# Kernel optimization log

Hardware: AMD Instinct MI355X
Metric: run time of the kernel (lower is better)

The kernel has to match this reference:

```python
import jax, jax.numpy as jnp
import numpy as np

N, TO, TI, H = 8, 2048, 2048, 128
MASK_FILL = -99999.0  # module uses -99999.0, not -inf


def setup_inputs() -> dict:
    key = jax.random.key(0)
    kq, kv, km = jax.random.split(key, 3)
    queries = jax.random.normal(kq, (N, TO, H), dtype=jnp.float32)
    values = jax.random.normal(kv, (N, TI, H), dtype=jnp.float32)
    # mask is applied to scores.view(-1, Ti) -> shape (N*To, Ti), True = masked
    mask = jax.random.randint(km, (N * TO, TI), 0, 2).astype(bool)
    return {"queries": queries, "values": values, "mask": mask}


def reference(queries, values, mask):
    n, to, h = queries.shape
    ti = values.shape[1]
    # N x To x Ti scores (no 1/sqrt(H) scaling in the original)
    scores = jnp.einsum("nth,nsh->nts", queries, values)
    scores = jnp.where(mask.reshape(n, to, ti), MASK_FILL, scores)
    attention_distribution = jax.nn.softmax(scores, axis=-1)
    attention_output = jnp.einsum("nts,nsh->nth", attention_distribution, values)
    return attention_output, attention_distribution
```

## Files before the change

kernel.cpp:

```cpp
#include <hip/hip_runtime.h>

#define NB  8
#define TOQ 2048
#define TIV 2048
#define HD  128

typedef float f32x4 __attribute__((ext_vector_type(4)));
typedef short s16x8 __attribute__((ext_vector_type(8)));
typedef unsigned short ushort8v __attribute__((ext_vector_type(8)));

__device__ __forceinline__ unsigned short f2bf(float f) {
    unsigned u = __float_as_uint(f);
    return (unsigned short)((u + 0x7FFFu + ((u >> 16) & 1u)) >> 16);
}
__device__ __forceinline__ float bf2f(unsigned short h) {
    return __uint_as_float(((unsigned)h) << 16);
}

__device__ __forceinline__ void split8(const float4 a, const float4 b,
                                       ushort8v& h, ushort8v& l) {
    const float x[8] = {a.x, a.y, a.z, a.w, b.x, b.y, b.z, b.w};
    #pragma unroll
    for (int j = 0; j < 8; ++j) {
        const unsigned short hi = f2bf(x[j]);
        h[j] = hi;
        l[j] = f2bf(x[j] - bf2f(hi));
    }
}

__global__ __launch_bounds__(256) void k0_vt(
    const float* __restrict__ V, unsigned short* __restrict__ VT)
{
    __shared__ unsigned short tile[64][68];
    const int n  = blockIdx.z;
    const int s0 = blockIdx.x * 64;
    const int h0 = blockIdx.y * 64;
    const int t  = threadIdx.x;

    #pragma unroll
    for (int it = 0; it < 4; ++it) {
        const int f = t + it * 256;
        const int r = f >> 4;
        const int c = f & 15;
        const float4 v = *(const float4*)&V[((size_t)(n * TIV + s0 + r)) * HD + h0 + 4 * c];
        tile[4 * c + 0][r] = f2bf(v.x);
        tile[4 * c + 1][r] = f2bf(v.y);
        tile[4 * c + 2][r] = f2bf(v.z);
        tile[4 * c + 3][r] = f2bf(v.w);
    }
    __syncthreads();

    #pragma unroll
    for (int it = 0; it < 2; ++it) {
        const int f  = t + it * 256;
        const int hh = f >> 3;
        const int sc = f & 7;
        ushort8v o;
        #pragma unroll
        for (int j = 0; j < 8; ++j) o[j] = tile[hh][8 * sc + j];
        *(ushort8v*)&VT[((size_t)(n * HD + h0 + hh)) * TIV + s0 + 8 * sc] = o;
    }
}

__global__ __launch_bounds__(256) void k1_mfma(
    const float* __restrict__ Q, const float* __restrict__ V,
    const int* __restrict__ M, float* __restrict__ E)
{
    __shared__ unsigned short qhi[128 * 32], qlo[128 * 32];
    __shared__ unsigned short vhi[128 * 32], vlo[128 * 32];

    const int n    = blockIdx.z;
    const int tt   = blockIdx.y * 128;
    const int ts   = blockIdx.x * 128;
    const int t    = threadIdx.x;
    const int lane = t & 63;
    const int wave = t >> 6;
    const int wr   = wave >> 1;
    const int wc   = wave & 1;
    const int lr   = lane & 15;
    const int kg   = lane >> 4;

    const float* Qb = Q + ((size_t)n * TOQ + tt) * HD;
    const float* Vb = V + ((size_t)n * TIV + ts) * HD;

    f32x4 acc[4][4];
    #pragma unroll
    for (int i = 0; i < 4; ++i)
        #pragma unroll
        for (int j = 0; j < 4; ++j) acc[i][j] = (f32x4)0.f;

    for (int h0 = 0; h0 < HD; h0 += 32) {
        #pragma unroll
        for (int it = 0; it < 2; ++it) {
            const int i   = t + it * 256;
            const int row = i >> 2;
            const int kb  = i & 3;
            const float* qs = Qb + (size_t)row * HD + h0 + kb * 8;
            const float* vs = Vb + (size_t)row * HD + h0 + kb * 8;
            const float4 q0 = *(const float4*)qs, q1 = *(const float4*)(qs + 4);
            const float4 v0 = *(const float4*)vs, v1 = *(const float4*)(vs + 4);
            ushort8v qh, ql, vh, vl;
            split8(q0, q1, qh, ql);
            split8(v0, v1, vh, vl);
            *(ushort8v*)(qhi + i * 8) = qh;
            *(ushort8v*)(qlo + i * 8) = ql;
            *(ushort8v*)(vhi + i * 8) = vh;
            *(ushort8v*)(vlo + i * 8) = vl;
        }
        __syncthreads();

        s16x8 aH[4], aL[4];
        #pragma unroll
        for (int fm = 0; fm < 4; ++fm) {
            const int off = (wr * 64 + fm * 16 + lr) * 32 + kg * 8;
            aH[fm] = *(const s16x8*)(qhi + off);
            aL[fm] = *(const s16x8*)(qlo + off);
        }
        #pragma unroll
        for (int fn = 0; fn < 4; ++fn) {
            const int off = (wc * 64 + fn * 16 + lr) * 32 + kg * 8;
            const s16x8 bH = *(const s16x8*)(vhi + off);
            const s16x8 bL = *(const s16x8*)(vlo + off);
            #pragma unroll
            for (int fm = 0; fm < 4; ++fm) {
                acc[fm][fn] = __builtin_amdgcn_mfma_f32_16x16x32_bf16(aH[fm], bH, acc[fm][fn], 0, 0, 0);
                acc[fm][fn] = __builtin_amdgcn_mfma_f32_16x16x32_bf16(aH[fm], bL, acc[fm][fn], 0, 0, 0);
                acc[fm][fn] = __builtin_amdgcn_mfma_f32_16x16x32_bf16(aL[fm], bH, acc[fm][fn], 0, 0, 0);
            }
        }
        __syncthreads();
    }

    #pragma unroll
    for (int fm = 0; fm < 4; ++fm) {
        #pragma unroll
        for (int fn = 0; fn < 4; ++fn) {
            #pragma unroll
            for (int ri = 0; ri < 4; ++ri) {
                const int r = tt + wr * 64 + fm * 16 + kg * 4 + ri;
                const int c = ts + wc * 64 + fn * 16 + lr;
                const size_t off = ((size_t)n * TOQ + r) * TIV + c;
                E[off] = M[off] ? 0.f : __expf(acc[fm][fn][ri]);
            }
        }
    }
}

__global__ __launch_bounds__(256) void k2_rowsum(
    const float* __restrict__ E, float* __restrict__ rec)
{
    const int row = blockIdx.x * 4 + (threadIdx.x >> 6);
    const int l   = threadIdx.x & 63;
    const float4* Er = (const float4*)(E + (size_t)row * TIV);
    float s = 0.f;
    #pragma unroll
    for (int k = 0; k < 8; ++k) {
        const float4 v = Er[l + 64 * k];
        s += (v.x + v.y) + (v.z + v.w);
    }
    #pragma unroll
    for (int off = 32; off > 0; off >>= 1) s += __shfl_down(s, off, 64);
    if (l == 0) rec[row] = 1.f / s;
}

__global__ __launch_bounds__(512) void k3_pv(
    float* EP,
    const unsigned short* __restrict__ VT,
    const float* __restrict__ rec, float* __restrict__ O)
{
    __shared__ float red[4][16][132];

    const int n    = blockIdx.y;
    const int r0   = blockIdx.x * 64;
    const int t    = threadIdx.x;
    const int wave = t >> 6;
    const int lane = t & 63;
    const int p    = wave >> 1;
    const int half = wave & 1;
    const int lr   = lane & 15;
    const int kg   = lane >> 4;

    const int rowg = r0 + p * 16 + lr;
    const float rc = rec[n * TOQ + rowg];
    float* Erow = EP + ((size_t)n * TOQ + rowg) * TIV;
    const unsigned short* VTb = VT + (size_t)n * HD * TIV;

    f32x4 acc[8];
    #pragma unroll
    for (int fn = 0; fn < 8; ++fn) acc[fn] = (f32x4)0.f;

    const int kbase = half * 1024 + kg * 8;

    #pragma unroll 2
    for (int k0 = 0; k0 < 1024; k0 += 32) {
        const int k = kbase + k0;
        const float4 e0 = *(const float4*)&Erow[k];
        const float4 e1 = *(const float4*)&Erow[k + 4];
        float4 p0, p1;
        p0.x = e0.x * rc; p0.y = e0.y * rc; p0.z = e0.z * rc; p0.w = e0.w * rc;
        p1.x = e1.x * rc; p1.y = e1.y * rc; p1.z = e1.z * rc; p1.w = e1.w * rc;
        *(float4*)&Erow[k]     = p0;
        *(float4*)&Erow[k + 4] = p1;

        s16x8 a;
        a[0] = (short)f2bf(p0.x); a[1] = (short)f2bf(p0.y);
        a[2] = (short)f2bf(p0.z); a[3] = (short)f2bf(p0.w);
        a[4] = (short)f2bf(p1.x); a[5] = (short)f2bf(p1.y);
        a[6] = (short)f2bf(p1.z); a[7] = (short)f2bf(p1.w);

        #pragma unroll
        for (int fn = 0; fn < 8; ++fn) {
            const s16x8 b = *(const s16x8*)&VTb[(size_t)(fn * 16 + lr) * TIV + k];
            acc[fn] = __builtin_amdgcn_mfma_f32_16x16x32_bf16(a, b, acc[fn], 0, 0, 0);
        }
    }

    if (half == 1) {
        #pragma unroll
        for (int fn = 0; fn < 8; ++fn)
            #pragma unroll
            for (int ri = 0; ri < 4; ++ri)
                red[p][kg * 4 + ri][fn * 16 + lr] = acc[fn][ri];
    }
    __syncthreads();
    if (half == 0) {
        #pragma unroll
        for (int fn = 0; fn < 8; ++fn) {
            #pragma unroll
            for (int ri = 0; ri < 4; ++ri) {
                const int orow = r0 + p * 16 + kg * 4 + ri;
                const float o = acc[fn][ri] + red[p][kg * 4 + ri][fn * 16 + lr];
                O[((size_t)n * TOQ + orow) * HD + fn * 16 + lr] = o;
            }
        }
    }
}

extern "C" void kernel_launch(void* const* d_in, const int* in_sizes, int n_in,
                              void* d_out, int out_size, void* d_ws, size_t ws_size,
                              hipStream_t stream)
{
    const float* Q = (const float*)d_in[0];
    const float* V = (const float*)d_in[1];
    const int*   M = (const int*)d_in[2];

    float* O = (float*)d_out;
    float* E = O + (size_t)NB * TOQ * HD;

    float*          recb = (float*)d_ws;
    unsigned short* VT   = (unsigned short*)((char*)d_ws + (1 << 16));

    k0_vt    <<<dim3(TIV / 64, HD / 64, NB), 256, 0, stream>>>(V, VT);
    k1_mfma  <<<dim3(TIV / 128, TOQ / 128, NB), 256, 0, stream>>>(Q, V, M, E);
    k2_rowsum<<<dim3(NB * TOQ / 4), 256, 0, stream>>>(E, recb);
    k3_pv    <<<dim3(TOQ / 64, NB), 512, 0, stream>>>(E, VT, recb, O);
}
```

Before: 198.0 us.

## Fuse row-sum partials into score kernel and split PV K-range four ways

The score kernel now accumulates per-row partial sums of the exponentials and writes 32 partials per row to workspace. The row-sum kernel then reduces those partials instead of re-reading the full 128MB exp matrix. The PV kernel processes 32 rows per block with four waves splitting the K range, which doubles the number of blocks, and reduces the partial results through shared memory. This removes a full pass over E in exchange for a small partials buffer and more shared-memory reduction work.

```diff
diff --git a/kernel.cpp b/kernel.cpp
--- a/kernel.cpp
+++ b/kernel.cpp
@@ -64,7 +64,8 @@
 
 __global__ __launch_bounds__(256) void k1_mfma(
     const float* __restrict__ Q, const float* __restrict__ V,
-    const int* __restrict__ M, float* __restrict__ E)
+    const int* __restrict__ M, float* __restrict__ E,
+    float* __restrict__ part)
 {
     __shared__ unsigned short qhi[128 * 32], qlo[128 * 32];
     __shared__ unsigned short vhi[128 * 32], vlo[128 * 32];
@@ -131,6 +132,12 @@
         __syncthreads();
     }
 
+    float rsum[4][4];
+    #pragma unroll
+    for (int fm = 0; fm < 4; ++fm)
+        #pragma unroll
+        for (int ri = 0; ri < 4; ++ri) rsum[fm][ri] = 0.f;
+
     #pragma unroll
     for (int fm = 0; fm < 4; ++fm) {
         #pragma unroll
@@ -140,43 +147,56 @@
                 const int r = tt + wr * 64 + fm * 16 + kg * 4 + ri;
                 const int c = ts + wc * 64 + fn * 16 + lr;
                 const size_t off = ((size_t)n * TOQ + r) * TIV + c;
-                E[off] = M[off] ? 0.f : __expf(acc[fm][fn][ri]);
+                const float e = M[off] ? 0.f : __expf(acc[fm][fn][ri]);
+                E[off] = e;
+                rsum[fm][ri] += e;
+            }
+        }
+    }
+    #pragma unroll
+    for (int fm = 0; fm < 4; ++fm) {
+        #pragma unroll
+        for (int ri = 0; ri < 4; ++ri) {
+            float s = rsum[fm][ri];
+            s += __shfl_xor(s, 1, 64);
+            s += __shfl_xor(s, 2, 64);
+            s += __shfl_xor(s, 4, 64);
+            s += __shfl_xor(s, 8, 64);
+            if (lr == 0) {
+                const int r = tt + wr * 64 + fm * 16 + kg * 4 + ri;
+                part[((size_t)n * TOQ + r) * 32 + blockIdx.x * 2 + wc] = s;
             }
         }
     }
 }
 
 __global__ __launch_bounds__(256) void k2_rowsum(
-    const float* __restrict__ E, float* __restrict__ rec)
-{
-    const int row = blockIdx.x * 4 + (threadIdx.x >> 6);
-    const int l   = threadIdx.x & 63;
-    const float4* Er = (const float4*)(E + (size_t)row * TIV);
+    const float* __restrict__ part, float* __restrict__ rec)
+{
+    const int row = blockIdx.x * 256 + threadIdx.x;
+    const float4* p4 = (const float4*)(part + (size_t)row * 32);
     float s = 0.f;
     #pragma unroll
-    for (int k = 0; k < 8; ++k) {
-        const float4 v = Er[l + 64 * k];
+    for (int i = 0; i < 8; ++i) {
+        const float4 v = p4[i];
         s += (v.x + v.y) + (v.z + v.w);
     }
-    #pragma unroll
-    for (int off = 32; off > 0; off >>= 1) s += __shfl_down(s, off, 64);
-    if (l == 0) rec[row] = 1.f / s;
+    rec[row] = 1.f / s;
 }
 
 __global__ __launch_bounds__(512) void k3_pv(
-    float* EP,
-    const unsigned short* __restrict__ VT,
+    float* __restrict__ EP, const unsigned short* __restrict__ VT,
     const float* __restrict__ rec, float* __restrict__ O)
 {
-    __shared__ float red[4][16][132];
+    __shared__ float red[2][3][16][132];
 
     const int n    = blockIdx.y;
-    const int r0   = blockIdx.x * 64;
+    const int r0   = blockIdx.x * 32;
     const int t    = threadIdx.x;
     const int wave = t >> 6;
     const int lane = t & 63;
-    const int p    = wave >> 1;
-    const int half = wave & 1;
+    const int p    = wave >> 2;
+    const int q    = wave & 3;
     const int lr   = lane & 15;
     const int kg   = lane >> 4;
 
@@ -189,10 +209,10 @@
     #pragma unroll
     for (int fn = 0; fn < 8; ++fn) acc[fn] = (f32x4)0.f;
 
-    const int kbase = half * 1024 + kg * 8;
+    const int kbase = q * 512 + kg * 8;
 
     #pragma unroll 2
-    for (int k0 = 0; k0 < 1024; k0 += 32) {
+    for (int k0 = 0; k0 < 512; k0 += 32) {
         const int k = kbase + k0;
         const float4 e0 = *(const float4*)&Erow[k];
         const float4 e1 = *(const float4*)&Erow[k + 4];
@@ -215,21 +235,24 @@
         }
     }
 
-    if (half == 1) {
+    if (q != 0) {
         #pragma unroll
         for (int fn = 0; fn < 8; ++fn)
             #pragma unroll
             for (int ri = 0; ri < 4; ++ri)
-                red[p][kg * 4 + ri][fn * 16 + lr] = acc[fn][ri];
+                red[p][q - 1][kg * 4 + ri][fn * 16 + lr] = acc[fn][ri];
     }
     __syncthreads();
-    if (half == 0) {
+    if (q == 0) {
         #pragma unroll
         for (int fn = 0; fn < 8; ++fn) {
             #pragma unroll
             for (int ri = 0; ri < 4; ++ri) {
                 const int orow = r0 + p * 16 + kg * 4 + ri;
-                const float o = acc[fn][ri] + red[p][kg * 4 + ri][fn * 16 + lr];
+                float o = acc[fn][ri];
+                o += red[p][0][kg * 4 + ri][fn * 16 + lr];
+                o += red[p][1][kg * 4 + ri][fn * 16 + lr];
+                o += red[p][2][kg * 4 + ri][fn * 16 + lr];
                 O[((size_t)n * TOQ + orow) * HD + fn * 16 + lr] = o;
             }
         }
@@ -248,10 +271,11 @@
     float* E = O + (size_t)NB * TOQ * HD;
 
     float*          recb = (float*)d_ws;
-    unsigned short* VT   = (unsigned short*)((char*)d_ws + (1 << 16));
+    float*          part = (float*)((char*)d_ws + (1 << 16));
+    unsigned short* VT   = (unsigned short*)((char*)d_ws + (1 << 16) + (NB * TOQ * 32 * 4));
 
     k0_vt    <<<dim3(TIV / 64, HD / 64, NB), 256, 0, stream>>>(V, VT);
-    k1_mfma  <<<dim3(TIV / 128, TOQ / 128, NB), 256, 0, stream>>>(Q, V, M, E);
-    k2_rowsum<<<dim3(NB * TOQ / 4), 256, 0, stream>>>(E, recb);
-    k3_pv    <<<dim3(TOQ / 64, NB), 512, 0, stream>>>(E, VT, recb, O);
-}
+    k1_mfma  <<<dim3(TIV / 128, TOQ / 128, NB), 256, 0, stream>>>(Q, V, M, E, part);
+    k2_rowsum<<<dim3(NB * TOQ / 256), 256, 0, stream>>>(part, recb);
+    k3_pv    <<<dim3(TOQ / 32, NB), 512, 0, stream>>>(E, VT, recb, O);
+}
```

Result: faster. 188.0 us (-5.0%).

## Store unnormalized exp scores as bf16 in-place and split PV reduction four ways

Applied to the files above, without the earlier changes.

The score kernel now writes exp(scores) as bf16 into the first half of each fp32 row of the output buffer, which halves the intermediate write and the row-sum read traffic. The PV kernel preloads a whole bf16 row segment into registers, syncs, then overwrites the row with normalized fp32 probabilities so the in-place aliasing stays safe. Work is split into four K-quarters per 16-row group with a larger shared-memory reduction, and blocks cover 32 rows instead of 64. In exchange, the attention distribution loses precision because it is rebuilt from bf16 exponentials, and register pressure rises from the 16-element preload buffer.

```diff
diff --git a/kernel.cpp b/kernel.cpp
--- a/kernel.cpp
+++ b/kernel.cpp
@@ -64,7 +64,7 @@
 
 __global__ __launch_bounds__(256) void k1_mfma(
     const float* __restrict__ Q, const float* __restrict__ V,
-    const int* __restrict__ M, float* __restrict__ E)
+    const int* __restrict__ M, float* __restrict__ Pf)
 {
     __shared__ unsigned short qhi[128 * 32], qlo[128 * 32];
     __shared__ unsigned short vhi[128 * 32], vlo[128 * 32];
@@ -139,74 +139,83 @@
             for (int ri = 0; ri < 4; ++ri) {
                 const int r = tt + wr * 64 + fm * 16 + kg * 4 + ri;
                 const int c = ts + wc * 64 + fn * 16 + lr;
-                const size_t off = ((size_t)n * TOQ + r) * TIV + c;
-                E[off] = M[off] ? 0.f : __expf(acc[fm][fn][ri]);
+                const size_t R   = (size_t)n * TOQ + r;
+                const size_t off = R * TIV + c;
+                unsigned short* Eu = (unsigned short*)(Pf + R * TIV);
+                Eu[c] = M[off] ? (unsigned short)0 : f2bf(__expf(acc[fm][fn][ri]));
             }
         }
     }
 }
 
 __global__ __launch_bounds__(256) void k2_rowsum(
-    const float* __restrict__ E, float* __restrict__ rec)
+    const float* __restrict__ Pf, float* __restrict__ rec)
 {
     const int row = blockIdx.x * 4 + (threadIdx.x >> 6);
     const int l   = threadIdx.x & 63;
-    const float4* Er = (const float4*)(E + (size_t)row * TIV);
+    const unsigned short* Eu = (const unsigned short*)(Pf + (size_t)row * TIV);
     float s = 0.f;
     #pragma unroll
-    for (int k = 0; k < 8; ++k) {
-        const float4 v = Er[l + 64 * k];
-        s += (v.x + v.y) + (v.z + v.w);
+    for (int kk = 0; kk < 4; ++kk) {
+        const ushort8v v = *(const ushort8v*)&Eu[(l + 64 * kk) * 8];
+        #pragma unroll
+        for (int j = 0; j < 8; ++j) s += bf2f(v[j]);
     }
     #pragma unroll
     for (int off = 32; off > 0; off >>= 1) s += __shfl_down(s, off, 64);
     if (l == 0) rec[row] = 1.f / s;
 }
 
-__global__ __launch_bounds__(512) void k3_pv(
-    float* EP,
-    const unsigned short* __restrict__ VT,
+__global__ __launch_bounds__(512, 4) void k3_pv(
+    float* __restrict__ Pf, const unsigned short* __restrict__ VT,
     const float* __restrict__ rec, float* __restrict__ O)
 {
-    __shared__ float red[4][16][132];
+    __shared__ float red[2][3][16][132];
 
     const int n    = blockIdx.y;
-    const int r0   = blockIdx.x * 64;
+    const int r0   = blockIdx.x * 32;
     const int t    = threadIdx.x;
     const int wave = t >> 6;
     const int lane = t & 63;
-    const int p    = wave >> 1;
-    const int half = wave & 1;
+    const int p    = wave >> 2;
+    const int q    = wave & 3;
     const int lr   = lane & 15;
     const int kg   = lane >> 4;
 
     const int rowg = r0 + p * 16 + lr;
     const float rc = rec[n * TOQ + rowg];
-    float* Erow = EP + ((size_t)n * TOQ + rowg) * TIV;
-    const unsigned short* VTb = VT + (size_t)n * HD * TIV;
+    float* Prow = Pf + ((size_t)n * TOQ + rowg) * TIV;
+    const unsigned short* Erow = (const unsigned short*)Prow;
+    const unsigned short* VTb  = VT + (size_t)n * HD * TIV;
+
+    ushort8v est[16];
+    #pragma unroll
+    for (int i = 0; i < 16; ++i)
+        est[i] = *(const ushort8v*)&Erow[q * 512 + i * 32 + kg * 8];
+
+    __syncthreads();
 
     f32x4 acc[8];
     #pragma unroll
     for (int fn = 0; fn < 8; ++fn) acc[fn] = (f32x4)0.f;
 
-    const int kbase = half * 1024 + kg * 8;
-
     #pragma unroll 2
-    for (int k0 = 0; k0 < 1024; k0 += 32) {
-        const int k = kbase + k0;
-        const float4 e0 = *(const float4*)&Erow[k];
-        const float4 e1 = *(const float4*)&Erow[k + 4];
+    for (int i = 0; i < 16; ++i) {
+        const int k = q * 512 + i * 32 + kg * 8;
+        const ushort8v ev = est[i];
+        float pv[8];
+        #pragma unroll
+        for (int j = 0; j < 8; ++j) pv[j] = bf2f(ev[j]) * rc;
+
         float4 p0, p1;
-        p0.x = e0.x * rc; p0.y = e0.y * rc; p0.z = e0.z * rc; p0.w = e0.w * rc;
-        p1.x = e1.x * rc; p1.y = e1.y * rc; p1.z = e1.z * rc; p1.w = e1.w * rc;
-        *(float4*)&Erow[k]     = p0;
-        *(float4*)&Erow[k + 4] = p1;
+        p0.x = pv[0]; p0.y = pv[1]; p0.z = pv[2]; p0.w = pv[3];
+        p1.x = pv[4]; p1.y = pv[5]; p1.z = pv[6]; p1.w = pv[7];
+        *(float4*)&Prow[k]     = p0;
+        *(float4*)&Prow[k + 4] = p1;
 
         s16x8 a;
-        a[0] = (short)f2bf(p0.x); a[1] = (short)f2bf(p0.y);
-        a[2] = (short)f2bf(p0.z); a[3] = (short)f2bf(p0.w);
-        a[4] = (short)f2bf(p1.x); a[5] = (short)f2bf(p1.y);
-        a[6] = (short)f2bf(p1.z); a[7] = (short)f2bf(p1.w);
+        #pragma unroll
+        for (int j = 0; j < 8; ++j) a[j] = (short)f2bf(pv[j]);
 
         #pragma unroll
         for (int fn = 0; fn < 8; ++fn) {
@@ -215,21 +224,24 @@
         }
     }
 
-    if (half == 1) {
+    if (q != 0) {
         #pragma unroll
         for (int fn = 0; fn < 8; ++fn)
             #pragma unroll
             for (int ri = 0; ri < 4; ++ri)
-                red[p][kg * 4 + ri][fn * 16 + lr] = acc[fn][ri];
+                red[p][q - 1][kg * 4 + ri][fn * 16 + lr] = acc[fn][ri];
     }
     __syncthreads();
-    if (half == 0) {
+    if (q == 0) {
         #pragma unroll
         for (int fn = 0; fn < 8; ++fn) {
             #pragma unroll
             for (int ri = 0; ri < 4; ++ri) {
                 const int orow = r0 + p * 16 + kg * 4 + ri;
-                const float o = acc[fn][ri] + red[p][kg * 4 + ri][fn * 16 + lr];
+                float o = acc[fn][ri];
+                o += red[p][0][kg * 4 + ri][fn * 16 + lr];
+                o += red[p][1][kg * 4 + ri][fn * 16 + lr];
+                o += red[p][2][kg * 4 + ri][fn * 16 + lr];
                 O[((size_t)n * TOQ + orow) * HD + fn * 16 + lr] = o;
             }
         }
@@ -244,14 +256,14 @@
     const float* V = (const float*)d_in[1];
     const int*   M = (const int*)d_in[2];
 
-    float* O = (float*)d_out;
-    float* E = O + (size_t)NB * TOQ * HD;
+    float* O  = (float*)d_out;
+    float* Pf = O + (size_t)NB * TOQ * HD;
 
     float*          recb = (float*)d_ws;
     unsigned short* VT   = (unsigned short*)((char*)d_ws + (1 << 16));
 
     k0_vt    <<<dim3(TIV / 64, HD / 64, NB), 256, 0, stream>>>(V, VT);
-    k1_mfma  <<<dim3(TIV / 128, TOQ / 128, NB), 256, 0, stream>>>(Q, V, M, E);
-    k2_rowsum<<<dim3(NB * TOQ / 4), 256, 0, stream>>>(E, recb);
-    k3_pv    <<<dim3(TOQ / 64, NB), 512, 0, stream>>>(E, VT, recb, O);
-}
+    k1_mfma  <<<dim3(TIV / 128, TOQ / 128, NB), 256, 0, stream>>>(Q, V, M, Pf);
+    k2_rowsum<<<dim3(NB * TOQ / 4), 256, 0, stream>>>(Pf, recb);
+    k3_pv    <<<dim3(TOQ / 32, NB), 512, 0, stream>>>(Pf, VT, recb, O);
+}
```

New measurement: 313.8 us. 58.5% more time.
